# Kernel optimization log

Hardware: AMD Instinct MI355X
Metric: run time of the kernel (lower is better)

The kernel has to match this reference:

```python
import jax, jax.numpy as jnp
import numpy as np

B, S, D, H = 2, 2048, 1024, 16
DH = D // H


def setup_inputs() -> dict:
    key = jax.random.key(0)
    ks = jax.random.split(key, 6)
    scale = 0.02
    X = jax.random.normal(ks[0], (B, S, D), dtype=jnp.float32)
    masks = jax.random.randint(ks[1], (B, S), 0, 2).astype(jnp.int32)
    Wq = jax.random.normal(ks[2], (D, D), dtype=jnp.float32) * scale
    Wk = jax.random.normal(ks[3], (D, D), dtype=jnp.float32) * scale
    Wv = jax.random.normal(ks[4], (D, D), dtype=jnp.float32) * scale
    Wo = jax.random.normal(ks[5], (D, D), dtype=jnp.float32) * scale
    return {"X": X, "masks": masks, "Wq": Wq, "Wk": Wk, "Wv": Wv, "Wo": Wo}


def reference(X, masks, Wq, Wk, Wv, Wo):
    b, s, d = X.shape
    masks_b = masks.astype(bool)                       # [B,S] key validity
    lookahead = jnp.triu(jnp.ones((s, s), dtype=bool), 1)  # [S,S] future positions
    pad = ~masks_b[:, None, :]                         # [B,1,S] -> invalid keys
    invalid = pad | lookahead[None, :, :]              # [B,S,S]
    valid = (~invalid)[:, None, :, :].astype(X.dtype)  # [B,1,S,S]

    def split_heads(Y):  # [B,S,D] -> [B,H,S,DH]
        return Y.reshape(b, s, H, DH).transpose(0, 2, 1, 3)

    Q = split_heads(X @ Wq.T)
    K = split_heads(X @ Wk.T)
    V = split_heads(X @ Wv.T)

    Qn = Q / jnp.sqrt(jnp.sum(Q * Q, axis=-1, keepdims=True))
    Kn = K / jnp.sqrt(jnp.sum(K * K, axis=-1, keepdims=True))

    scores = jnp.einsum('bhqd,bhkd->bhqk', Qn, Kn)     # cosine similarities
    att = jax.nn.relu(scores) * valid                  # relu + causal/pad mask
    ctx = jnp.einsum('bhqk,bhkd->bhqd', att, V)
    ctx = ctx * masks_b[:, None, :, None].astype(X.dtype)  # zero padded queries

    out = ctx.transpose(0, 2, 1, 3).reshape(b, s, d)
    return out @ Wo.T
```

## Files before the change

kernel.cpp:

```cpp
#include <hip/hip_runtime.h>
#include <hip/hip_bf16.h>

#define BB 2
#define SS 2048
#define DD 1024
#define HH 16
#define MMR (BB*SS)
#define ND3 3072

typedef __hip_bfloat16 bf;
typedef __bf16 bf16x8 __attribute__((ext_vector_type(8)));
typedef float f32x4 __attribute__((ext_vector_type(4)));
typedef float f32x16 __attribute__((ext_vector_type(16)));

#define VMCNT(n) asm volatile("s_waitcnt vmcnt(" #n ")" ::: "memory")

__device__ __forceinline__ f32x4 mfma16(bf16x8 a, bf16x8 b, f32x4 c) {
    return __builtin_amdgcn_mfma_f32_16x16x32_bf16(a, b, c, 0, 0, 0);
}
__device__ __forceinline__ f32x16 mfma32(bf16x8 a, bf16x8 b, f32x16 c) {
    return __builtin_amdgcn_mfma_f32_32x32x16_bf16(a, b, c, 0, 0, 0);
}
__device__ __forceinline__ unsigned cvt_pk_bf16(float lo, float hi) {
    unsigned r;
    asm("v_cvt_pk_bf16_f32 %0, %1, %2" : "=v"(r) : "v"(lo), "v"(hi));
    return r;
}
__device__ __forceinline__ void pl32swap(unsigned& a, unsigned& b) {
    asm("v_permlane32_swap_b32 %0, %1" : "+v"(a), "+v"(b));
}
__device__ __forceinline__ void glds16(const bf* g, bf* l) {
    __builtin_amdgcn_global_load_lds(
        (const __attribute__((address_space(1))) void*)g,
        (__attribute__((address_space(3))) void*)l,
        16, 0, 0);
}

__global__ __launch_bounds__(256) void k_convert(const float* __restrict__ X,
                                                 const float* __restrict__ Wq,
                                                 const float* __restrict__ Wk,
                                                 const float* __restrict__ Wv,
                                                 const float* __restrict__ Wo,
                                                 bf* __restrict__ Xb,
                                                 bf* __restrict__ Wqkv,
                                                 bf* __restrict__ Wob) {
    const int bid = blockIdx.x;
    const float* src;
    bf* dst;
    int off;
    if (bid < 4096) {
        src = X; dst = Xb; off = bid;
    } else {
        const int r = (bid - 4096) >> 10;
        src = (r == 0) ? Wq : (r == 1) ? Wk : (r == 2) ? Wv : Wo;
        dst = (r < 3) ? (Wqkv + (size_t)r * 1048576) : Wob;
        off = (bid - 4096) & 1023;
    }
    const int j = (off * 256 + threadIdx.x) * 4;
    float4 v = *(const float4*)(src + j);
    bf tmp[4];
    tmp[0] = __float2bfloat16(v.x);
    tmp[1] = __float2bfloat16(v.y);
    tmp[2] = __float2bfloat16(v.z);
    tmp[3] = __float2bfloat16(v.w);
    *(uint2*)(dst + j) = *(const uint2*)tmp;
}

template<int MODE, int BM, int BN>
__global__ __launch_bounds__(256) void k_gemm(const bf* __restrict__ A,
                                              const bf* __restrict__ Bt,
                                              float* __restrict__ Cf,
                                              const int* __restrict__ masks,
                                              bf* __restrict__ Qn,
                                              bf* __restrict__ Kn,
                                              bf* __restrict__ Vt,
                                              int nx, int N, int K) {
    constexpr int MF = BM / 32;
    constexpr int RA = BM / 64;
    constexpr int RB = BN / 64;
    __shared__ __align__(16) bf Asm[3][BM * 32];
    __shared__ __align__(16) bf Bsm[3][BN * 32];
    const int tid = threadIdx.x;
    const int w = tid >> 6, lane = tid & 63, g = lane >> 4, rl = lane & 15;
    const int cpx = gridDim.x >> 3;
    const int swz = (blockIdx.x & 7) * cpx + (blockIdx.x >> 3);
    const int m0 = (swz / nx) * BM, n0 = (swz % nx) * BN;
    const int wr = (w >> 1) * (MF * 16), wc = (w & 1) * 64;
    const int lrow = lane >> 2, lseg = lane & 3;

    f32x4 acc[MF][4] = {};
    const bf* Ap = A + (size_t)m0 * K;
    const bf* Bp = Bt + (size_t)n0 * K;

    auto stage = [&](int bi, int k0) {
#pragma unroll
        for (int u = 0; u < RA; ++u)
            glds16(Ap + (size_t)(u * 64 + w * 16 + lrow) * K + k0 + lseg * 8,
                   &Asm[bi][(u * 64 + w * 16) * 32]);
#pragma unroll
        for (int u = 0; u < RB; ++u)
            glds16(Bp + (size_t)(u * 64 + w * 16 + lrow) * K + k0 + lseg * 8,
                   &Bsm[bi][(u * 64 + w * 16) * 32]);
    };

    const int T = K >> 5;
    stage(0, 0);
    stage(1, 32);
    int cur = 0, nxt = 2;
    for (int t = 0; t < T; ++t) {
        __builtin_amdgcn_sched_barrier(0);
        if (t < T - 1) {
            if constexpr (RA + RB == 4) VMCNT(4); else VMCNT(3);
        } else {
            VMCNT(0);
        }
        __builtin_amdgcn_s_barrier();
        __builtin_amdgcn_sched_barrier(0);
        if (t + 2 < T) stage(nxt, (t + 2) * 32);

        const bf* Ab = Asm[cur];
        const bf* Bb = Bsm[cur];
        bf16x8 af[MF], bfr[4];
#pragma unroll
        for (int m = 0; m < MF; ++m)
            af[m] = __builtin_bit_cast(bf16x8, *(const int4*)&Ab[(wr + m * 16 + rl) * 32 + g * 8]);
#pragma unroll
        for (int n = 0; n < 4; ++n)
            bfr[n] = __builtin_bit_cast(bf16x8, *(const int4*)&Bb[(wc + n * 16 + rl) * 32 + g * 8]);
#pragma unroll
        for (int m = 0; m < MF; ++m)
#pragma unroll
            for (int n = 0; n < 4; ++n)
                acc[m][n] = mfma16(af[m], bfr[n], acc[m][n]);

        cur = (cur == 2) ? 0 : cur + 1;
        nxt = (nxt == 2) ? 0 : nxt + 1;
    }

    if constexpr (MODE == 0) {
#pragma unroll
        for (int m = 0; m < MF; ++m)
#pragma unroll
            for (int n = 0; n < 4; ++n)
#pragma unroll
                for (int ri = 0; ri < 4; ++ri)
                    Cf[(size_t)(m0 + wr + m * 16 + g * 4 + ri) * N + n0 + wc + n * 16 + rl] =
                        acc[m][n][ri];
    } else {
        const int ncol0 = n0 + wc;
        if (ncol0 < 2048) {
            bf* dst = (ncol0 < 1024) ? Qn : Kn;
            const int h2 = (ncol0 >> 6) & 15;
#pragma unroll
            for (int m = 0; m < MF; ++m) {
#pragma unroll
                for (int ri = 0; ri < 4; ++ri) {
                    const int row = m0 + wr + m * 16 + g * 4 + ri;
                    float ss = 0.f;
#pragma unroll
                    for (int n = 0; n < 4; ++n) ss += acc[m][n][ri] * acc[m][n][ri];
#pragma unroll
                    for (int d = 1; d < 16; d <<= 1) ss += __shfl_xor(ss, d, 64);
                    const float sc = rsqrtf(ss) * (masks[row] ? 1.0f : 0.0f);
                    const int b = row >> 11, s = row & 2047;
                    const size_t base = ((size_t)(b * HH + h2) * SS + s) * 64;
#pragma unroll
                    for (int n = 0; n < 4; ++n)
                        dst[base + n * 16 + rl] = __float2bfloat16(acc[m][n][ri] * sc);
                }
            }
        } else {
            const int h2 = (ncol0 - 2048) >> 6;
            const int b = (m0 + wr) >> 11;
            const int sb = ((m0 + wr) & 2047) + g * 4;
#pragma unroll
            for (int m = 0; m < MF; ++m)
#pragma unroll
                for (int n = 0; n < 4; ++n) {
                    const int d = n * 16 + rl;
                    bf t4[4];
#pragma unroll
                    for (int ri = 0; ri < 4; ++ri) t4[ri] = __float2bfloat16(acc[m][n][ri]);
                    *(uint2*)&Vt[((size_t)(b * HH + h2) * 64 + d) * SS + sb + m * 16] =
                        *(uint2*)t4;
                }
        }
    }
}

__global__ __launch_bounds__(256) void k_attn(const bf* __restrict__ Qn,
                                              const bf* __restrict__ Kn,
                                              const bf* __restrict__ Vt,
                                              bf* __restrict__ Ctx) {
    __shared__ __align__(16) bf Ksm[2][64 * 64];
    __shared__ __align__(16) bf Vsm[2][64 * 64];

    const int idx = blockIdx.x;
    const int qt = 31 - (idx >> 5);
    const int by = idx & 31;
    const int b = by >> 4, h = by & 15;
    const int tid = threadIdx.x;
    const int w = tid >> 6, lane = tid & 63;
    const int l31 = lane & 31, hl = lane >> 5;
    const int qh = w >> 1;
    const int kp = w & 1;
    const int qw = qt * 64 + qh * 32;
    const int qg = qw + l31;

    const bf* Qp = Qn + (size_t)by * SS * 64;
    const bf* Kp = Kn + (size_t)by * SS * 64;
    const bf* Vp = Vt + (size_t)by * 64 * SS;

    bf16x8 aqs[4];
#pragma unroll
    for (int st = 0; st < 4; ++st)
        aqs[st] = __builtin_bit_cast(bf16x8,
            *(const int4*)(Qp + (size_t)(qw + l31) * 64 + st * 16 + hl * 8));

    const int srow = lane >> 3;
    const int sblk = (lane & 7) ^ srow;

    auto stage = [&](int buf, int k0) {
#pragma unroll
        for (int u = 0; u < 2; ++u) {
            const int c = w * 2 + u;
            const int row = c * 8 + srow;
            glds16(Kp + (size_t)(k0 + row) * 64 + sblk * 8, &Ksm[buf][c * 512]);
            glds16(Vp + (size_t)row * SS + k0 + sblk * 8, &Vsm[buf][c * 512]);
        }
    };

    f32x16 accd[2] = {};

    stage(0, 0);
    __syncthreads();
    int cur = 0;
    for (int t = 0; t <= qt; ++t) {
        if (t < qt) stage(cur ^ 1, (t + 1) * 64);
        const int kbase = t * 64 + kp * 32;
        if (kbase <= qw + 31) {
            f32x16 pc = {};
#pragma unroll
            for (int st = 0; st < 4; ++st) {
                const int r = kp * 32 + l31;
                bf16x8 ak = __builtin_bit_cast(bf16x8,
                    *(const int4*)&Ksm[cur][r * 64 + (((2 * st + hl) ^ (r & 7)) << 3)]);
                pc = mfma32(ak, aqs[st], pc);
            }
            const bool dg = (kbase + 31 > qw);
            float pv[16];
#pragma unroll
            for (int m2 = 0; m2 < 16; ++m2) {
                float v = fmaxf(pc[m2], 0.0f);
                if (dg) {
                    const int kg = kbase + (m2 & 3) + 8 * (m2 >> 2) + 4 * hl;
                    if (kg > qg) v = 0.0f;
                }
                pv[m2] = v;
            }
            unsigned P[8];
#pragma unroll
            for (int m2 = 0; m2 < 8; ++m2) P[m2] = cvt_pk_bf16(pv[2 * m2], pv[2 * m2 + 1]);
            pl32swap(P[0], P[2]);
            pl32swap(P[1], P[3]);
            pl32swap(P[4], P[6]);
            pl32swap(P[5], P[7]);
#pragma unroll
            for (int s = 0; s < 2; ++s) {
                uint4 pw = {P[4 * s + 0], P[4 * s + 1], P[4 * s + 2], P[4 * s + 3]};
                bf16x8 pa = __builtin_bit_cast(bf16x8, pw);
#pragma unroll
                for (int dt = 0; dt < 2; ++dt) {
                    const int d = dt * 32 + l31;
                    const int slot = kp * 4 + s * 2 + hl;
                    bf16x8 bv = __builtin_bit_cast(bf16x8,
                        *(const int4*)&Vsm[cur][d * 64 + ((slot ^ (d & 7)) << 3)]);
                    accd[dt] = mfma32(pa, bv, accd[dt]);
                }
            }
        }
        __syncthreads();
        cur ^= 1;
    }

    float* red = (float*)&Ksm[0][0];
    if (kp == 1) {
#pragma unroll
        for (int dt = 0; dt < 2; ++dt)
#pragma unroll
            for (int m2 = 0; m2 < 16; ++m2)
                red[qh * 2048 + (dt * 16 + m2) * 64 + lane] = accd[dt][m2];
    }
    __syncthreads();
    if (kp == 0) {
#pragma unroll
        for (int dt = 0; dt < 2; ++dt)
#pragma unroll
            for (int m2 = 0; m2 < 16; ++m2) {
                const float v = accd[dt][m2] + red[qh * 2048 + (dt * 16 + m2) * 64 + lane];
                const int q = qw + (m2 & 3) + 8 * (m2 >> 2) + 4 * hl;
                const int d = dt * 32 + l31;
                Ctx[(size_t)(b * SS + q) * DD + h * 64 + d] = __float2bfloat16(v);
            }
    }
}

extern "C" void kernel_launch(void* const* d_in, const int* in_sizes, int n_in,
                              void* d_out, int out_size, void* d_ws, size_t ws_size,
                              hipStream_t stream) {
    const float* X  = (const float*)d_in[0];
    const int* masks = (const int*)d_in[1];
    const float* Wq = (const float*)d_in[2];
    const float* Wk = (const float*)d_in[3];
    const float* Wv = (const float*)d_in[4];
    const float* Wo = (const float*)d_in[5];
    float* out = (float*)d_out;
    char* ws = (char*)d_ws;

    const size_t MB = 1024 * 1024;
    bf* Xb   = (bf*)(ws);
    bf* Wqkv = (bf*)(ws + 8  * MB);
    bf* Wob  = (bf*)(ws + 14 * MB);
    bf* Qn   = (bf*)(ws + 16 * MB);
    bf* Kn   = (bf*)(ws + 24 * MB);
    bf* Vt   = (bf*)(ws + 32 * MB);
    bf* Ctx  = (bf*)(ws + 40 * MB);

    k_convert<<<8192, 256, 0, stream>>>(X, Wq, Wk, Wv, Wo, Xb, Wqkv, Wob);

    k_gemm<1, 128, 128><<<(ND3 / 128) * (MMR / 128), 256, 0, stream>>>(
        Xb, Wqkv, nullptr, masks, Qn, Kn, Vt, ND3 / 128, ND3, DD);

    k_attn<<<1024, 256, 0, stream>>>(Qn, Kn, Vt, Ctx);

    k_gemm<0, 64, 128><<<(DD / 128) * (MMR / 64), 256, 0, stream>>>(
        Ctx, Wob, out, nullptr, nullptr, nullptr, nullptr, DD / 128, DD, DD);
}
```

Baseline: 102.5 us.

## Swizzle GEMM LDS tiles, triple-buffer attention K/V, add MFMA priority hints

The GEMM kernel now XOR-swizzles the 16-byte segment position in its shared-memory A/B tiles, both when staging from global memory and when reading fragments, to reduce LDS bank conflicts. The attention kernel moves from double to triple buffering of K/V tiles, prefetching two tiles ahead. It replaces the per-iteration __syncthreads with a vmcnt wait plus a single barrier. MFMA sections in both kernels are wrapped in s_setprio to favour matrix-core issue. This costs more LDS per attention block, which may lower occupancy, and relies on exact vmcnt counts being correct.

```diff
diff --git a/kernel.cpp b/kernel.cpp
--- a/kernel.cpp
+++ b/kernel.cpp
@@ -87,6 +87,7 @@
     const int m0 = (swz / nx) * BM, n0 = (swz % nx) * BN;
     const int wr = (w >> 1) * (MF * 16), wc = (w & 1) * 64;
     const int lrow = lane >> 2, lseg = lane & 3;
+    const int xseg = lseg ^ ((lrow >> 1) & 3);
 
     f32x4 acc[MF][4] = {};
     const bf* Ap = A + (size_t)m0 * K;
@@ -95,11 +96,11 @@
     auto stage = [&](int bi, int k0) {
 #pragma unroll
         for (int u = 0; u < RA; ++u)
-            glds16(Ap + (size_t)(u * 64 + w * 16 + lrow) * K + k0 + lseg * 8,
+            glds16(Ap + (size_t)(u * 64 + w * 16 + lrow) * K + k0 + xseg * 8,
                    &Asm[bi][(u * 64 + w * 16) * 32]);
 #pragma unroll
         for (int u = 0; u < RB; ++u)
-            glds16(Bp + (size_t)(u * 64 + w * 16 + lrow) * K + k0 + lseg * 8,
+            glds16(Bp + (size_t)(u * 64 + w * 16 + lrow) * K + k0 + xseg * 8,
                    &Bsm[bi][(u * 64 + w * 16) * 32]);
     };
 
@@ -122,16 +123,24 @@
         const bf* Bb = Bsm[cur];
         bf16x8 af[MF], bfr[4];
 #pragma unroll
-        for (int m = 0; m < MF; ++m)
-            af[m] = __builtin_bit_cast(bf16x8, *(const int4*)&Ab[(wr + m * 16 + rl) * 32 + g * 8]);
-#pragma unroll
-        for (int n = 0; n < 4; ++n)
-            bfr[n] = __builtin_bit_cast(bf16x8, *(const int4*)&Bb[(wc + n * 16 + rl) * 32 + g * 8]);
+        for (int m = 0; m < MF; ++m) {
+            const int row = wr + m * 16 + rl;
+            af[m] = __builtin_bit_cast(bf16x8,
+                *(const int4*)&Ab[row * 32 + (g ^ ((row >> 1) & 3)) * 8]);
+        }
+#pragma unroll
+        for (int n = 0; n < 4; ++n) {
+            const int row = wc + n * 16 + rl;
+            bfr[n] = __builtin_bit_cast(bf16x8,
+                *(const int4*)&Bb[row * 32 + (g ^ ((row >> 1) & 3)) * 8]);
+        }
+        __builtin_amdgcn_s_setprio(1);
 #pragma unroll
         for (int m = 0; m < MF; ++m)
 #pragma unroll
             for (int n = 0; n < 4; ++n)
                 acc[m][n] = mfma16(af[m], bfr[n], acc[m][n]);
+        __builtin_amdgcn_s_setprio(0);
 
         cur = (cur == 2) ? 0 : cur + 1;
         nxt = (nxt == 2) ? 0 : nxt + 1;
@@ -192,8 +201,8 @@
                                               const bf* __restrict__ Kn,
                                               const bf* __restrict__ Vt,
                                               bf* __restrict__ Ctx) {
-    __shared__ __align__(16) bf Ksm[2][64 * 64];
-    __shared__ __align__(16) bf Vsm[2][64 * 64];
+    __shared__ __align__(16) bf Ksm[3][64 * 64];
+    __shared__ __align__(16) bf Vsm[3][64 * 64];
 
     const int idx = blockIdx.x;
     const int qt = 31 - (idx >> 5);
@@ -233,13 +242,19 @@
     f32x16 accd[2] = {};
 
     stage(0, 0);
-    __syncthreads();
-    int cur = 0;
+    stage(1, 64);
+    int cur = 0, nxt = 2;
     for (int t = 0; t <= qt; ++t) {
-        if (t < qt) stage(cur ^ 1, (t + 1) * 64);
+        __builtin_amdgcn_sched_barrier(0);
+        if (t < qt) { VMCNT(4); } else { VMCNT(0); }
+        __builtin_amdgcn_s_barrier();
+        __builtin_amdgcn_sched_barrier(0);
+        if (t + 2 <= qt) stage(nxt, (t + 2) * 64);
+
         const int kbase = t * 64 + kp * 32;
         if (kbase <= qw + 31) {
             f32x16 pc = {};
+            __builtin_amdgcn_s_setprio(1);
 #pragma unroll
             for (int st = 0; st < 4; ++st) {
                 const int r = kp * 32 + l31;
@@ -247,6 +262,7 @@
                     *(const int4*)&Ksm[cur][r * 64 + (((2 * st + hl) ^ (r & 7)) << 3)]);
                 pc = mfma32(ak, aqs[st], pc);
             }
+            __builtin_amdgcn_s_setprio(0);
             const bool dg = (kbase + 31 > qw);
             float pv[16];
 #pragma unroll
@@ -265,6 +281,7 @@
             pl32swap(P[1], P[3]);
             pl32swap(P[4], P[6]);
             pl32swap(P[5], P[7]);
+            __builtin_amdgcn_s_setprio(1);
 #pragma unroll
             for (int s = 0; s < 2; ++s) {
                 uint4 pw = {P[4 * s + 0], P[4 * s + 1], P[4 * s + 2], P[4 * s + 3]};
@@ -278,11 +295,14 @@
                     accd[dt] = mfma32(pa, bv, accd[dt]);
                 }
             }
-        }
-        __syncthreads();
-        cur ^= 1;
-    }
-
+            __builtin_amdgcn_s_setprio(0);
+        }
+
+        cur = (cur == 2) ? 0 : cur + 1;
+        nxt = (nxt == 2) ? 0 : nxt + 1;
+    }
+
+    __syncthreads();
     float* red = (float*)&Ksm[0][0];
     if (kp == 1) {
 #pragma unroll
```

Result: slower. 104.9 us (+2.3%).
